# Performance work log

Hardware: AMD Instinct MI355X
Metric: run time of the kernel (lower is better)

The kernel has to match this reference:

```python
import jax, jax.numpy as jnp
import numpy as np

HEADS = 8
DIM_HEAD = 64
DIM = 512
CTX_DIM = 512
INNER = HEADS * DIM_HEAD  # 512
EPS = 1e-5


def layernorm(x, g):
    # repo-style LayerNorm: learnable gain g only, no bias, biased variance
    mean = jnp.mean(x, axis=-1, keepdims=True)
    var = jnp.var(x, axis=-1, keepdims=True)
    return (x - mean) * jax.lax.rsqrt(var + EPS) * g


def setup_inputs() -> dict:
    key = jax.random.key(0)
    ks = jax.random.split(key, 8)
    b, n, m = 2, 4096, 4096
    x = jax.random.normal(ks[0], (b, n, DIM), dtype=jnp.float32)
    context = jax.random.normal(ks[1], (b, m, CTX_DIM), dtype=jnp.float32)
    mask = jax.random.bernoulli(ks[2], 0.9, (b, m))  # bool [b, m]
    # parameters
    g_x = jnp.ones((DIM,), dtype=jnp.float32)
    null_kv = jax.random.normal(ks[3], (2, DIM_HEAD), dtype=jnp.float32)
    Wq = jax.random.normal(ks[4], (DIM, INNER), dtype=jnp.float32) * (DIM ** -0.5)
    Wkv = jax.random.normal(ks[5], (CTX_DIM, 2 * INNER), dtype=jnp.float32) * (CTX_DIM ** -0.5)
    Wo = jax.random.normal(ks[6], (INNER, DIM), dtype=jnp.float32) * (INNER ** -0.5)
    g_out = jnp.ones((DIM,), dtype=jnp.float32)
    return {"x": x, "context": context, "mask": mask, "g_x": g_x,
            "null_kv": null_kv, "Wq": Wq, "Wkv": Wkv, "Wo": Wo, "g_out": g_out}


def reference(x, context, mask, g_x, null_kv, Wq, Wkv, Wo, g_out):
    b, n, _ = x.shape
    m = context.shape[1]
    scale = DIM_HEAD ** (-0.5)  # cosine_sim=False

    xn = layernorm(x, g_x)
    ctx = context  # norm_context=False -> Identity

    q = (xn @ Wq).reshape(b, n, HEADS, DIM_HEAD)          # b n h d
    kv = (ctx @ Wkv).reshape(b, m, 2, HEADS, DIM_HEAD)     # b m 2 h d
    k, v = kv[:, :, 0], kv[:, :, 1]                        # b m h d

    # prepend the null kv token (shared across b, h)
    nk = jnp.broadcast_to(null_kv[0], (b, 1, HEADS, DIM_HEAD))
    nv = jnp.broadcast_to(null_kv[1], (b, 1, HEADS, DIM_HEAD))
    k = jnp.concatenate([nk, k], axis=1)                   # b (m+1) h d
    v = jnp.concatenate([nv, v], axis=1)

    s = jnp.sqrt(jnp.float32(scale))
    q = q * s
    k = k * s

    sim = jnp.einsum('bihd,bjhd->bhij', q, k)              # b h n (m+1)
    max_neg = -jnp.finfo(sim.dtype).max
    full_mask = jnp.pad(mask, ((0, 0), (1, 0)), constant_values=True)  # null token visible
    sim = jnp.where(full_mask[:, None, None, :], sim, max_neg)

    attn = jax.nn.softmax(sim.astype(jnp.float32), axis=-1).astype(sim.dtype)
    out = jnp.einsum('bhij,bjhd->bihd', attn, v).reshape(b, n, INNER)
    out = out @ Wo
    return layernorm(out, g_out)
```

## Files before the change

### kernel.cpp

```cpp
#include <hip/hip_runtime.h>
#include <cfloat>

typedef unsigned short u16;
typedef unsigned int u32;
typedef __bf16 v8bf16 __attribute__((ext_vector_type(8)));
typedef float v4f32 __attribute__((ext_vector_type(4)));
typedef float v16f32 __attribute__((ext_vector_type(16)));

#define MPAD 4224
#define QKS 0.42466090f
#define GRPS 1024

__device__ __forceinline__ u16 f2bf(float f) {
  union { float f; u32 u; } v; v.f = f;
  u32 u = v.u;
  u32 r = (u + 0x7FFFu + ((u >> 16) & 1u)) >> 16;
  return (u16)r;
}

__device__ __forceinline__ u32 pkbf(float lo, float hi) {
  union { float f; u32 u; } a, c;
  a.f = lo; c.f = hi;
  return __builtin_amdgcn_perm(c.u, a.u, 0x07060302);
}

__device__ __forceinline__ float asf(u32 u) {
  union { u32 u; float f; } v; v.u = u; return v.f;
}

__global__ __launch_bounds__(256) void transpose_cast3(const float* __restrict__ Wq,
    const float* __restrict__ Wkv, const float* __restrict__ Wo,
    u16* __restrict__ WqT, u16* __restrict__ WkvT, u16* __restrict__ WoT) {
  __shared__ float tile[32][33];
  int bb = blockIdx.x;
  const float* in; u16* out; int N; float scale; int base;
  if (bb < 256)      { in = Wq;  out = WqT;  N = 512;  scale = QKS; base = bb; }
  else if (bb < 768) { in = Wkv; out = WkvT; N = 1024; scale = 1.f; base = bb - 256; }
  else               { in = Wo;  out = WoT;  N = 512;  scale = 1.f; base = bb - 768; }
  const int K = 512;
  int ntiles = N >> 5;
  int bx = base % ntiles, by = base / ntiles;
  int n0 = bx * 32, k0 = by * 32;
  int c = threadIdx.x & 31, r8 = threadIdx.x >> 5;
#pragma unroll
  for (int i = 0; i < 4; i++) {
    int r = r8 + i * 8;
    tile[r][c] = in[(size_t)(k0 + r) * N + n0 + c];
  }
  __syncthreads();
#pragma unroll
  for (int i = 0; i < 4; i++) {
    int r = r8 + i * 8;
    out[(size_t)(n0 + r) * K + k0 + c] = f2bf(tile[c][r] * scale);
  }
}

__global__ __launch_bounds__(256) void ln_to_bf16(const float* __restrict__ in,
    const float* __restrict__ g, u16* __restrict__ out) {
  int lane = threadIdx.x & 63, w = threadIdx.x >> 6;
  int row = blockIdx.x * 4 + w;
  const float* p = in + (size_t)row * 512 + lane * 8;
  float4 f0 = *(const float4*)p;
  float4 f1 = *(const float4*)(p + 4);
  float v[8] = {f0.x, f0.y, f0.z, f0.w, f1.x, f1.y, f1.z, f1.w};
  float sum = 0.f, sq = 0.f;
#pragma unroll
  for (int i = 0; i < 8; i++) { sum += v[i]; sq += v[i] * v[i]; }
#pragma unroll
  for (int m = 1; m < 64; m <<= 1) { sum += __shfl_xor(sum, m); sq += __shfl_xor(sq, m); }
  float mean = sum * (1.f / 512.f);
  float var = sq * (1.f / 512.f) - mean * mean;
  float rstd = rsqrtf(var + 1e-5f);
  const float* gp = g + lane * 8;
  u16 o[8];
#pragma unroll
  for (int i = 0; i < 8; i++) o[i] = f2bf((v[i] - mean) * rstd * gp[i]);
  *(uint4*)&out[(size_t)row * 512 + lane * 8] = *(uint4*)o;
}

__global__ __launch_bounds__(256) void ln_to_f32(const float* __restrict__ in,
    const float* __restrict__ g, float* __restrict__ out) {
  int lane = threadIdx.x & 63, w = threadIdx.x >> 6;
  int row = blockIdx.x * 4 + w;
  const float* p = in + (size_t)row * 512 + lane * 8;
  float4 f0 = *(const float4*)p;
  float4 f1 = *(const float4*)(p + 4);
  float v[8] = {f0.x, f0.y, f0.z, f0.w, f1.x, f1.y, f1.z, f1.w};
  float sum = 0.f, sq = 0.f;
#pragma unroll
  for (int i = 0; i < 8; i++) { sum += v[i]; sq += v[i] * v[i]; }
#pragma unroll
  for (int m = 1; m < 64; m <<= 1) { sum += __shfl_xor(sum, m); sq += __shfl_xor(sq, m); }
  float mean = sum * (1.f / 512.f);
  float var = sq * (1.f / 512.f) - mean * mean;
  float rstd = rsqrtf(var + 1e-5f);
  const float* gp = g + lane * 8;
  float o[8];
#pragma unroll
  for (int i = 0; i < 8; i++) o[i] = (v[i] - mean) * rstd * gp[i];
  float* q = out + (size_t)row * 512 + lane * 8;
  *(float4*)q = make_float4(o[0], o[1], o[2], o[3]);
  *(float4*)(q + 4) = make_float4(o[4], o[5], o[6], o[7]);
}

__global__ __launch_bounds__(256) void cast_f32_bf16(const float4* __restrict__ in,
    u16* __restrict__ out, int n4) {
  int i = blockIdx.x * 256 + threadIdx.x;
  if (i >= n4) return;
  float4 f = in[i];
  u16 o[4] = {f2bf(f.x), f2bf(f.y), f2bf(f.z), f2bf(f.w)};
  *(uint2*)&out[i * 4] = *(uint2*)o;
}

__global__ void detect_mask_dtype(const unsigned char* __restrict__ m, int* __restrict__ flag) {
  int i = blockIdx.x * 256 + threadIdx.x;
  if (i < 8192 && (i & 3) && m[i]) atomicOr(flag, 1);
}

__global__ void build_maskpad(const void* __restrict__ mask, const int* __restrict__ flag,
    float* __restrict__ mp) {
  int i = blockIdx.x * 256 + threadIdx.x;
  if (i >= 2 * MPAD) return;
  int b = i / MPAD, p = i - b * MPAD;
  float v;
  if (p == 0) v = 0.f;
  else if (p <= 4096) {
    int j = b * 4096 + (p - 1);
    int on = (*flag) ? (((const unsigned char*)mask)[j] != 0)
                     : (((const int*)mask)[j] != 0);
    v = on ? 0.f : -1e38f;
  } else v = -1e38f;
  mp[i] = v;
}

__global__ __launch_bounds__(256) void fill_extras(const float* __restrict__ nullkv,
    u16* __restrict__ KVt) {
  int bh = blockIdx.x, tid = threadIdx.x;
  size_t tb64 = ((size_t)bh * 66 + 64) * 8192;
  uint4 z = make_uint4(0, 0, 0, 0);
  for (int i = tid; i < 2048; i += 256)
    *(uint4*)&KVt[tb64 + (size_t)i * 8] = z;
  size_t tb0 = (size_t)bh * 66 * 8192;
  if (tid < 64) {
    int d = tid;
    KVt[tb0 + (size_t)(d >> 3) * 512 + (d & 7)] = f2bf(nullkv[d] * QKS);
    KVt[tb0 + 4096 + (size_t)d * 8] = f2bf(nullkv[64 + d]);
  }
}

__global__ __launch_bounds__(256) void gemm_bf16(const u16* __restrict__ A,
    const u16* __restrict__ Bt, u16* __restrict__ outb, float* __restrict__ outf,
    u16* __restrict__ KVt, int Ncols, int mode) {
  __shared__ __attribute__((aligned(16))) u16 As[128 * 32];
  __shared__ __attribute__((aligned(16))) u16 Bs[64 * 32];
  int tiles_n = Ncols >> 6;
  int n0 = (blockIdx.x % tiles_n) * 64;
  int m0 = (blockIdx.x / tiles_n) * 128;
  int tid = threadIdx.x;
  int lane = tid & 63, w = tid >> 6, quad = lane >> 4, l15 = lane & 15;
  int srow = tid >> 2, scol = (tid & 3) * 8;
  v4f32 acc[2][4];
#pragma unroll
  for (int i = 0; i < 2; i++)
#pragma unroll
    for (int j = 0; j < 4; j++) acc[i][j] = (v4f32){0.f, 0.f, 0.f, 0.f};

  for (int k0 = 0; k0 < 512; k0 += 32) {
    __syncthreads();
    __builtin_amdgcn_global_load_lds((const u32*)&A[(size_t)(m0 + srow) * 512 + k0 + scol],
                                     (u32*)&As[tid * 8], 16, 0, 0);
    __builtin_amdgcn_global_load_lds((const u32*)&A[(size_t)(m0 + 64 + srow) * 512 + k0 + scol],
                                     (u32*)&As[64 * 32 + tid * 8], 16, 0, 0);
    __builtin_amdgcn_global_load_lds((const u32*)&Bt[(size_t)(n0 + srow) * 512 + k0 + scol],
                                     (u32*)&Bs[tid * 8], 16, 0, 0);
    __syncthreads();
    v8bf16 af[2], bf[4];
#pragma unroll
    for (int i = 0; i < 2; i++)
      af[i] = *(const v8bf16*)&As[(w * 32 + i * 16 + l15) * 32 + quad * 8];
#pragma unroll
    for (int j = 0; j < 4; j++)
      bf[j] = *(const v8bf16*)&Bs[(j * 16 + l15) * 32 + quad * 8];
#pragma unroll
    for (int i = 0; i < 2; i++)
#pragma unroll
      for (int j = 0; j < 4; j++)
        acc[i][j] = __builtin_amdgcn_mfma_f32_16x16x32_bf16(af[i], bf[j], acc[i][j], 0, 0, 0);
  }
#pragma unroll
  for (int i = 0; i < 2; i++) {
    int rbase = m0 + w * 32 + i * 16 + quad * 4;
#pragma unroll
    for (int j = 0; j < 4; j++) {
      int col = n0 + j * 16 + l15;
#pragma unroll
      for (int r = 0; r < 4; r++) {
        float v = acc[i][j][r];
        int row = rbase + r;
        if (mode == 0) {
          outb[(size_t)row * 512 + col] = f2bf(v);
        } else if (mode == 2) {
          outf[(size_t)row * 512 + col] = v;
        } else {
          int b2 = row >> 12, mr = row & 4095;
          int kk = mr + 1, kt = kk >> 6, kl = kk & 63;
          int kvsel = col >> 9, hh = (col >> 6) & 7, d = col & 63;
          size_t tb = ((size_t)(b2 * 8 + hh) * 66 + kt) * 8192;
          if (kvsel == 0) {
            int chunk = (((d >> 4) * 2 + ((d >> 3) & 1)) * 2 + (kl >> 5)) * 32 + (kl & 31);
            KVt[tb + (size_t)chunk * 8 + (d & 7)] = f2bf(v * QKS);
          } else {
            int chunk = (((kl >> 4) * 2 + ((kl >> 3) & 1)) * 2 + (d >> 5)) * 32 + (d & 31);
            KVt[tb + 4096 + (size_t)chunk * 8 + (kl & 7)] = f2bf(v);
          }
        }
      }
    }
  }
}

__global__ __launch_bounds__(256, 2) void attn_kernel(const u16* __restrict__ q,
    const u16* __restrict__ KVt, const float* __restrict__ maskbias,
    u32* __restrict__ Opart, float* __restrict__ lbuf) {
  int bid = blockIdx.x;
  int qt = bid & 15, bhs = bid >> 4;
  int s_p = bhs & 1, bh = bhs >> 1;
  int b = bh >> 3, hh = bh & 7;
  int tid = threadIdx.x, lane = tid & 63, w = tid >> 6;
  int m31 = lane & 31, h = (lane >> 5) & 1;
  int grp = (bh * 16 + qt) * 4 + w;
  int q0 = qt * 256 + w * 64;

  v8bf16 qf[2][4];
#pragma unroll
  for (int qg = 0; qg < 2; qg++) {
    const u16* qp = q + (size_t)(b * 4096 + q0 + qg * 32 + m31) * 512 + hh * 64 + h * 8;
#pragma unroll
    for (int ks = 0; ks < 4; ks++) qf[qg][ks] = *(const v8bf16*)&qp[ks * 16];
  }

  v16f32 acc[2][2];
#pragma unroll
  for (int qg = 0; qg < 2; qg++)
#pragma unroll
    for (int db = 0; db < 2; db++)
#pragma unroll
      for (int i = 0; i < 16; i++) acc[qg][db][i] = 0.f;
  float l_st[2] = {0.f, 0.f};

  const u16* kvb = KVt + (size_t)bh * 66 * 8192 + (size_t)(h * 64 + m31) * 8;
  const float* mg = maskbias + b * MPAD;
  int kt0 = s_p * 33;

  for (int kt = kt0; kt < kt0 + 33; ++kt) {
    const u16* tb = kvb + (size_t)kt * 8192;
    v8bf16 kf[4][2];
#pragma unroll
    for (int ks = 0; ks < 4; ks++)
#pragma unroll
      for (int kc = 0; kc < 2; kc++)
        kf[ks][kc] = *(const v8bf16*)&tb[ks * 1024 + kc * 256];
    v16f32 bias_s[2];
#pragma unroll
    for (int kc = 0; kc < 2; kc++)
#pragma unroll
      for (int gg = 0; gg < 4; gg++) {
        float4 bv = *(const float4*)&mg[kt * 64 + kc * 32 + gg * 8 + h * 4];
        bias_s[kc][gg * 4 + 0] = bv.x;
        bias_s[kc][gg * 4 + 1] = bv.y;
        bias_s[kc][gg * 4 + 2] = bv.z;
        bias_s[kc][gg * 4 + 3] = bv.w;
      }

    v8bf16 pf[2][4];
    {
      v16f32 s[2];
#pragma unroll
      for (int kc = 0; kc < 2; kc++) {
        s[kc] = bias_s[kc];
#pragma unroll
        for (int ks = 0; ks < 4; ks++)
          s[kc] = __builtin_amdgcn_mfma_f32_32x32x16_bf16(kf[ks][kc], qf[0][ks], s[kc], 0, 0, 0);
      }
      float rsum = 0.f;
#pragma unroll
      for (int kc = 0; kc < 2; kc++)
#pragma unroll
        for (int i = 0; i < 16; i++) {
          float pv = __builtin_amdgcn_exp2f(s[kc][i]);
          s[kc][i] = pv;
          rsum += pv;
        }
      rsum += __shfl_xor(rsum, 32);
      l_st[0] += rsum;
#pragma unroll
      for (int kc = 0; kc < 2; kc++)
#pragma unroll
        for (int s16 = 0; s16 < 2; s16++) {
          u32 plo0 = pkbf(s[kc][s16 * 8 + 0], s[kc][s16 * 8 + 1]);
          u32 plo1 = pkbf(s[kc][s16 * 8 + 2], s[kc][s16 * 8 + 3]);
          u32 phi0 = pkbf(s[kc][s16 * 8 + 4], s[kc][s16 * 8 + 5]);
          u32 phi1 = pkbf(s[kc][s16 * 8 + 6], s[kc][s16 * 8 + 7]);
          u32 snd0 = h ? plo0 : phi0;
          u32 snd1 = h ? plo1 : phi1;
          u32 rcv0 = (u32)__shfl_xor((int)snd0, 32);
          u32 rcv1 = (u32)__shfl_xor((int)snd1, 32);
          union { u32 u[4]; v8bf16 v; } pu;
          pu.u[0] = h ? rcv0 : plo0;
          pu.u[1] = h ? rcv1 : plo1;
          pu.u[2] = h ? phi0 : rcv0;
          pu.u[3] = h ? phi1 : rcv1;
          pf[0][kc * 2 + s16] = pu.v;
        }
    }
    {
#pragma unroll
      for (int kc = 0; kc < 2; kc++)
#pragma unroll
        for (int ks = 0; ks < 4; ks++)
          bias_s[kc] = __builtin_amdgcn_mfma_f32_32x32x16_bf16(kf[ks][kc], qf[1][ks], bias_s[kc], 0, 0, 0);
      float rsum = 0.f;
#pragma unroll
      for (int kc = 0; kc < 2; kc++)
#pragma unroll
        for (int i = 0; i < 16; i++) {
          float pv = __builtin_amdgcn_exp2f(bias_s[kc][i]);
          bias_s[kc][i] = pv;
          rsum += pv;
        }
      rsum += __shfl_xor(rsum, 32);
      l_st[1] += rsum;
#pragma unroll
      for (int kc = 0; kc < 2; kc++)
#pragma unroll
        for (int s16 = 0; s16 < 2; s16++) {
          u32 plo0 = pkbf(bias_s[kc][s16 * 8 + 0], bias_s[kc][s16 * 8 + 1]);
          u32 plo1 = pkbf(bias_s[kc][s16 * 8 + 2], bias_s[kc][s16 * 8 + 3]);
          u32 phi0 = pkbf(bias_s[kc][s16 * 8 + 4], bias_s[kc][s16 * 8 + 5]);
          u32 phi1 = pkbf(bias_s[kc][s16 * 8 + 6], bias_s[kc][s16 * 8 + 7]);
          u32 snd0 = h ? plo0 : phi0;
          u32 snd1 = h ? plo1 : phi1;
          u32 rcv0 = (u32)__shfl_xor((int)snd0, 32);
          u32 rcv1 = (u32)__shfl_xor((int)snd1, 32);
          union { u32 u[4]; v8bf16 v; } pu;
          pu.u[0] = h ? rcv0 : plo0;
          pu.u[1] = h ? rcv1 : plo1;
          pu.u[2] = h ? phi0 : rcv0;
          pu.u[3] = h ? phi1 : rcv1;
          pf[1][kc * 2 + s16] = pu.v;
        }
    }

    v8bf16 vf[4][2];
#pragma unroll
    for (int jb = 0; jb < 4; jb++)
#pragma unroll
      for (int db = 0; db < 2; db++)
        vf[jb][db] = *(const v8bf16*)&tb[4096 + jb * 1024 + db * 256];

#pragma unroll
    for (int qg = 0; qg < 2; qg++)
#pragma unroll
      for (int jb = 0; jb < 4; jb++)
#pragma unroll
        for (int db = 0; db < 2; db++)
          acc[qg][db] = __builtin_amdgcn_mfma_f32_32x32x16_bf16(vf[jb][db], pf[qg][jb], acc[qg][db], 0, 0, 0);
  }

  size_t ob = (size_t)(s_p * GRPS + grp) * 2048;
#pragma unroll
  for (int qg = 0; qg < 2; qg++)
#pragma unroll
    for (int db = 0; db < 2; db++)
#pragma unroll
      for (int rp = 0; rp < 8; rp++)
        Opart[ob + qg * 1024 + (size_t)(db * 8 + rp) * 64 + lane] =
            pkbf(acc[qg][db][2 * rp], acc[qg][db][2 * rp + 1]);
  if (h == 0) {
    lbuf[(size_t)(s_p * GRPS + grp) * 64 + m31] = l_st[0];
    lbuf[(size_t)(s_p * GRPS + grp) * 64 + 32 + m31] = l_st[1];
  }
}

__global__ __launch_bounds__(256) void attn_combine(const u32* __restrict__ Opart,
    const float* __restrict__ lbuf, u16* __restrict__ attnO) {
  __shared__ __attribute__((aligned(16))) u16 tl[4][2176];
  int tid = threadIdx.x, lane = tid & 63, w4 = tid >> 6;
  int m31 = lane & 31, h = (lane >> 5) & 1;
  int gq = blockIdx.x * 4 + w4;
  int qg = gq & 1, grp = gq >> 1;
  int w = grp & 3, qt = (grp >> 2) & 15, bh = grp >> 6;
  int b = bh >> 3, hh = bh & 7;

  float l0 = lbuf[(size_t)grp * 64 + qg * 32 + m31];
  float l1 = lbuf[(size_t)(GRPS + grp) * 64 + qg * 32 + m31];
  float inv = 1.f / (l0 + l1);

#pragma unroll
  for (int db = 0; db < 2; db++)
#pragma unroll
    for (int rp = 0; rp < 8; rp++) {
      u32 a = Opart[(size_t)grp * 2048 + qg * 1024 + (db * 8 + rp) * 64 + lane];
      u32 c = Opart[(size_t)(GRPS + grp) * 2048 + qg * 1024 + (db * 8 + rp) * 64 + lane];
      float fe = (asf(a << 16) + asf(c << 16)) * inv;
      float fo = (asf(a & 0xFFFF0000u) + asf(c & 0xFFFF0000u)) * inv;
      int reg = 2 * rp;
      int d0 = (reg & 3) + 8 * (reg >> 2) + 4 * h + 32 * db;
      *(u32*)&tl[w4][m31 * 68 + d0] = pkbf(fe, fo);
    }
  __builtin_amdgcn_s_waitcnt(0);
  int q0 = qt * 256 + w * 64 + qg * 32;
#pragma unroll
  for (int t2 = 0; t2 < 4; t2++) {
    int row = t2 * 8 + (lane >> 3), ch = lane & 7;
    uint4 val = *(uint4*)&tl[w4][row * 68 + ch * 8];
    *(uint4*)&attnO[(size_t)(b * 4096 + q0 + row) * 512 + hh * 64 + ch * 8] = val;
  }
}

extern "C" void kernel_launch(void* const* d_in, const int* in_sizes, int n_in,
                              void* d_out, int out_size, void* d_ws, size_t ws_size,
                              hipStream_t stream) {
  const float* x       = (const float*)d_in[0];
  const float* context = (const float*)d_in[1];
  const void*  mask    = d_in[2];
  const float* g_x     = (const float*)d_in[3];
  const float* null_kv = (const float*)d_in[4];
  const float* Wq      = (const float*)d_in[5];
  const float* Wkv     = (const float*)d_in[6];
  const float* Wo      = (const float*)d_in[7];
  const float* g_out   = (const float*)d_in[8];

  char* w = (char*)d_ws;
  size_t off = 0;
  auto alloc = [&](size_t bytes) { size_t o = off; off = (off + bytes + 255) & ~(size_t)255; return o; };

  u16* WqT    = (u16*)(w + alloc((size_t)512 * 512 * 2));
  u16* WkvT   = (u16*)(w + alloc((size_t)1024 * 512 * 2));
  u16* WoT    = (u16*)(w + alloc((size_t)512 * 512 * 2));
  float* mp   = (float*)(w + alloc((size_t)2 * MPAD * 4));
  int* flag   = (int*)(w + alloc(256));
  u16* KVt    = (u16*)(w + alloc((size_t)16 * 66 * 8192 * 2));
  u16* qb     = (u16*)(w + alloc((size_t)8192 * 512 * 2));
  u16* aO     = (u16*)(w + alloc((size_t)8192 * 512 * 2));
  size_t xn_off = alloc((size_t)8192 * 512 * 2);
  size_t cb_off = alloc((size_t)8192 * 512 * 2);
  float* lbb  = (float*)(w + alloc((size_t)2 * GRPS * 64 * 4));
  u16* xn   = (u16*)(w + xn_off);
  u16* cb   = (u16*)(w + cb_off);
  u32* Opart = (u32*)(w + xn_off);
  float* OP  = (float*)(w + xn_off);

  hipMemsetAsync(flag, 0, 4, stream);
  detect_mask_dtype<<<32, 256, 0, stream>>>((const unsigned char*)mask, flag);
  build_maskpad<<<(2 * MPAD + 255) / 256, 256, 0, stream>>>(mask, flag, mp);

  transpose_cast3<<<1024, 256, 0, stream>>>(Wq, Wkv, Wo, WqT, WkvT, WoT);

  ln_to_bf16<<<2048, 256, 0, stream>>>(x, g_x, xn);
  cast_f32_bf16<<<4096, 256, 0, stream>>>((const float4*)context, cb, 8192 * 512 / 4);
  fill_extras<<<16, 256, 0, stream>>>(null_kv, KVt);

  gemm_bf16<<<(8192 / 128) * (512 / 64), 256, 0, stream>>>(xn, WqT, qb, nullptr, nullptr, 512, 0);
  gemm_bf16<<<(8192 / 128) * (1024 / 64), 256, 0, stream>>>(cb, WkvT, nullptr, nullptr, KVt, 1024, 1);

  attn_kernel<<<512, 256, 0, stream>>>(qb, KVt, mp, Opart, lbb);
  attn_combine<<<512, 256, 0, stream>>>(Opart, lbb, aO);

  gemm_bf16<<<(8192 / 128) * (512 / 64), 256, 0, stream>>>(aO, WoT, nullptr, OP, nullptr, 512, 2);
  ln_to_f32<<<2048, 256, 0, stream>>>(OP, g_out, (float*)d_out);
}
```

Before: 272.9 us.

## Enlarge GEMM tiles, software-pipeline attention K loads, use permlane32 swaps

The GEMM moves from 128x64 to 128x128 tiles with a 2x2 wave layout, which improves reuse of the A and B tiles and halves the block count. The attention loop now prefetches the next K tile and mask bias while it computes the current one. It also interleaves the QK MFMAs for the two query groups with the exp and pack steps. Predicated shfl_xor exchanges are replaced by v_permlane32_swap instructions. Together these aim to hide load latency and cut cross-lane overhead, at the cost of higher register pressure and possible occupancy loss.

```diff
diff --git a/kernel.cpp b/kernel.cpp
--- a/kernel.cpp
+++ b/kernel.cpp
@@ -26,6 +26,34 @@
 
 __device__ __forceinline__ float asf(u32 u) {
   union { u32 u; float f; } v; v.u = u; return v.f;
+}
+
+__device__ __forceinline__ void exppack2(v16f32& sA, v16f32& sB, float& lst,
+                                         v8bf16 pf[4]) {
+  float rsum = 0.f;
+#pragma unroll
+  for (int i = 0; i < 16; i++) { float p = __builtin_amdgcn_exp2f(sA[i]); sA[i] = p; rsum += p; }
+#pragma unroll
+  for (int i = 0; i < 16; i++) { float p = __builtin_amdgcn_exp2f(sB[i]); sB[i] = p; rsum += p; }
+  float a2 = rsum, b2 = rsum;
+  asm("v_permlane32_swap_b32 %0, %1" : "+v"(a2), "+v"(b2));
+  lst += a2 + b2;
+#pragma unroll
+  for (int kc = 0; kc < 2; kc++) {
+    v16f32& s = kc ? sB : sA;
+#pragma unroll
+    for (int s16 = 0; s16 < 2; s16++) {
+      u32 w0 = pkbf(s[s16 * 8 + 0], s[s16 * 8 + 1]);
+      u32 w1 = pkbf(s[s16 * 8 + 2], s[s16 * 8 + 3]);
+      u32 w2 = pkbf(s[s16 * 8 + 4], s[s16 * 8 + 5]);
+      u32 w3 = pkbf(s[s16 * 8 + 6], s[s16 * 8 + 7]);
+      asm("v_permlane32_swap_b32 %0, %1" : "+v"(w0), "+v"(w2));
+      asm("v_permlane32_swap_b32 %0, %1" : "+v"(w1), "+v"(w3));
+      union { u32 u[4]; v8bf16 v; } pu;
+      pu.u[0] = w0; pu.u[1] = w1; pu.u[2] = w2; pu.u[3] = w3;
+      pf[kc * 2 + s16] = pu.v;
+    }
+  }
 }
 
 __global__ __launch_bounds__(256) void transpose_cast3(const float* __restrict__ Wq,
@@ -152,16 +180,17 @@
     const u16* __restrict__ Bt, u16* __restrict__ outb, float* __restrict__ outf,
     u16* __restrict__ KVt, int Ncols, int mode) {
   __shared__ __attribute__((aligned(16))) u16 As[128 * 32];
-  __shared__ __attribute__((aligned(16))) u16 Bs[64 * 32];
-  int tiles_n = Ncols >> 6;
-  int n0 = (blockIdx.x % tiles_n) * 64;
+  __shared__ __attribute__((aligned(16))) u16 Bs[128 * 32];
+  int tiles_n = Ncols >> 7;
+  int n0 = (blockIdx.x % tiles_n) * 128;
   int m0 = (blockIdx.x / tiles_n) * 128;
   int tid = threadIdx.x;
   int lane = tid & 63, w = tid >> 6, quad = lane >> 4, l15 = lane & 15;
+  int wr = w >> 1, wc = w & 1;
   int srow = tid >> 2, scol = (tid & 3) * 8;
-  v4f32 acc[2][4];
-#pragma unroll
-  for (int i = 0; i < 2; i++)
+  v4f32 acc[4][4];
+#pragma unroll
+  for (int i = 0; i < 4; i++)
 #pragma unroll
     for (int j = 0; j < 4; j++) acc[i][j] = (v4f32){0.f, 0.f, 0.f, 0.f};
 
@@ -173,26 +202,28 @@
                                      (u32*)&As[64 * 32 + tid * 8], 16, 0, 0);
     __builtin_amdgcn_global_load_lds((const u32*)&Bt[(size_t)(n0 + srow) * 512 + k0 + scol],
                                      (u32*)&Bs[tid * 8], 16, 0, 0);
+    __builtin_amdgcn_global_load_lds((const u32*)&Bt[(size_t)(n0 + 64 + srow) * 512 + k0 + scol],
+                                     (u32*)&Bs[64 * 32 + tid * 8], 16, 0, 0);
     __syncthreads();
-    v8bf16 af[2], bf[4];
-#pragma unroll
-    for (int i = 0; i < 2; i++)
-      af[i] = *(const v8bf16*)&As[(w * 32 + i * 16 + l15) * 32 + quad * 8];
+    v8bf16 af[4], bf[4];
+#pragma unroll
+    for (int i = 0; i < 4; i++)
+      af[i] = *(const v8bf16*)&As[(wr * 64 + i * 16 + l15) * 32 + quad * 8];
 #pragma unroll
     for (int j = 0; j < 4; j++)
-      bf[j] = *(const v8bf16*)&Bs[(j * 16 + l15) * 32 + quad * 8];
-#pragma unroll
-    for (int i = 0; i < 2; i++)
+      bf[j] = *(const v8bf16*)&Bs[(wc * 64 + j * 16 + l15) * 32 + quad * 8];
+#pragma unroll
+    for (int i = 0; i < 4; i++)
 #pragma unroll
       for (int j = 0; j < 4; j++)
         acc[i][j] = __builtin_amdgcn_mfma_f32_16x16x32_bf16(af[i], bf[j], acc[i][j], 0, 0, 0);
   }
 #pragma unroll
-  for (int i = 0; i < 2; i++) {
-    int rbase = m0 + w * 32 + i * 16 + quad * 4;
+  for (int i = 0; i < 4; i++) {
+    int rbase = m0 + wr * 64 + i * 16 + quad * 4;
 #pragma unroll
     for (int j = 0; j < 4; j++) {
-      int col = n0 + j * 16 + l15;
+      int col = n0 + wc * 64 + j * 16 + l15;
 #pragma unroll
       for (int r = 0; r < 4; r++) {
         float v = acc[i][j][r];
@@ -252,103 +283,36 @@
   const float* mg = maskbias + b * MPAD;
   int kt0 = s_p * 33;
 
+  v8bf16 kf[4][2];
+  v16f32 bs0, bs1;
+  {
+    const u16* tb0 = kvb + (size_t)kt0 * 8192;
+#pragma unroll
+    for (int ks = 0; ks < 4; ks++)
+#pragma unroll
+      for (int kc = 0; kc < 2; kc++)
+        kf[ks][kc] = *(const v8bf16*)&tb0[ks * 1024 + kc * 256];
+#pragma unroll
+    for (int gg = 0; gg < 4; gg++) {
+      float4 b0 = *(const float4*)&mg[kt0 * 64 + gg * 8 + h * 4];
+      float4 b1 = *(const float4*)&mg[kt0 * 64 + 32 + gg * 8 + h * 4];
+      bs0[gg * 4 + 0] = b0.x; bs0[gg * 4 + 1] = b0.y; bs0[gg * 4 + 2] = b0.z; bs0[gg * 4 + 3] = b0.w;
+      bs1[gg * 4 + 0] = b1.x; bs1[gg * 4 + 1] = b1.y; bs1[gg * 4 + 2] = b1.z; bs1[gg * 4 + 3] = b1.w;
+    }
+  }
+
   for (int kt = kt0; kt < kt0 + 33; ++kt) {
     const u16* tb = kvb + (size_t)kt * 8192;
-    v8bf16 kf[4][2];
-#pragma unroll
-    for (int ks = 0; ks < 4; ks++)
-#pragma unroll
-      for (int kc = 0; kc < 2; kc++)
-        kf[ks][kc] = *(const v8bf16*)&tb[ks * 1024 + kc * 256];
-    v16f32 bias_s[2];
-#pragma unroll
-    for (int kc = 0; kc < 2; kc++)
-#pragma unroll
-      for (int gg = 0; gg < 4; gg++) {
-        float4 bv = *(const float4*)&mg[kt * 64 + kc * 32 + gg * 8 + h * 4];
-        bias_s[kc][gg * 4 + 0] = bv.x;
-        bias_s[kc][gg * 4 + 1] = bv.y;
-        bias_s[kc][gg * 4 + 2] = bv.z;
-        bias_s[kc][gg * 4 + 3] = bv.w;
-      }
+    int ktn = (kt + 1 < kt0 + 33) ? kt + 1 : kt0;
+    const u16* tbn = kvb + (size_t)ktn * 8192;
 
     v8bf16 pf[2][4];
-    {
-      v16f32 s[2];
-#pragma unroll
-      for (int kc = 0; kc < 2; kc++) {
-        s[kc] = bias_s[kc];
-#pragma unroll
-        for (int ks = 0; ks < 4; ks++)
-          s[kc] = __builtin_amdgcn_mfma_f32_32x32x16_bf16(kf[ks][kc], qf[0][ks], s[kc], 0, 0, 0);
-      }
-      float rsum = 0.f;
-#pragma unroll
-      for (int kc = 0; kc < 2; kc++)
-#pragma unroll
-        for (int i = 0; i < 16; i++) {
-          float pv = __builtin_amdgcn_exp2f(s[kc][i]);
-          s[kc][i] = pv;
-          rsum += pv;
-        }
-      rsum += __shfl_xor(rsum, 32);
-      l_st[0] += rsum;
-#pragma unroll
-      for (int kc = 0; kc < 2; kc++)
-#pragma unroll
-        for (int s16 = 0; s16 < 2; s16++) {
-          u32 plo0 = pkbf(s[kc][s16 * 8 + 0], s[kc][s16 * 8 + 1]);
-          u32 plo1 = pkbf(s[kc][s16 * 8 + 2], s[kc][s16 * 8 + 3]);
-          u32 phi0 = pkbf(s[kc][s16 * 8 + 4], s[kc][s16 * 8 + 5]);
-          u32 phi1 = pkbf(s[kc][s16 * 8 + 6], s[kc][s16 * 8 + 7]);
-          u32 snd0 = h ? plo0 : phi0;
-          u32 snd1 = h ? plo1 : phi1;
-          u32 rcv0 = (u32)__shfl_xor((int)snd0, 32);
-          u32 rcv1 = (u32)__shfl_xor((int)snd1, 32);
-          union { u32 u[4]; v8bf16 v; } pu;
-          pu.u[0] = h ? rcv0 : plo0;
-          pu.u[1] = h ? rcv1 : plo1;
-          pu.u[2] = h ? phi0 : rcv0;
-          pu.u[3] = h ? phi1 : rcv1;
-          pf[0][kc * 2 + s16] = pu.v;
-        }
-    }
-    {
-#pragma unroll
-      for (int kc = 0; kc < 2; kc++)
-#pragma unroll
-        for (int ks = 0; ks < 4; ks++)
-          bias_s[kc] = __builtin_amdgcn_mfma_f32_32x32x16_bf16(kf[ks][kc], qf[1][ks], bias_s[kc], 0, 0, 0);
-      float rsum = 0.f;
-#pragma unroll
-      for (int kc = 0; kc < 2; kc++)
-#pragma unroll
-        for (int i = 0; i < 16; i++) {
-          float pv = __builtin_amdgcn_exp2f(bias_s[kc][i]);
-          bias_s[kc][i] = pv;
-          rsum += pv;
-        }
-      rsum += __shfl_xor(rsum, 32);
-      l_st[1] += rsum;
-#pragma unroll
-      for (int kc = 0; kc < 2; kc++)
-#pragma unroll
-        for (int s16 = 0; s16 < 2; s16++) {
-          u32 plo0 = pkbf(bias_s[kc][s16 * 8 + 0], bias_s[kc][s16 * 8 + 1]);
-          u32 plo1 = pkbf(bias_s[kc][s16 * 8 + 2], bias_s[kc][s16 * 8 + 3]);
-          u32 phi0 = pkbf(bias_s[kc][s16 * 8 + 4], bias_s[kc][s16 * 8 + 5]);
-          u32 phi1 = pkbf(bias_s[kc][s16 * 8 + 6], bias_s[kc][s16 * 8 + 7]);
-          u32 snd0 = h ? plo0 : phi0;
-          u32 snd1 = h ? plo1 : phi1;
-          u32 rcv0 = (u32)__shfl_xor((int)snd0, 32);
-          u32 rcv1 = (u32)__shfl_xor((int)snd1, 32);
-          union { u32 u[4]; v8bf16 v; } pu;
-          pu.u[0] = h ? rcv0 : plo0;
-          pu.u[1] = h ? rcv1 : plo1;
-          pu.u[2] = h ? phi0 : rcv0;
-          pu.u[3] = h ? phi1 : rcv1;
-          pf[1][kc * 2 + s16] = pu.v;
-        }
+
+    v16f32 s0 = bs0, s1 = bs1;
+#pragma unroll
+    for (int ks = 0; ks < 4; ks++) {
+      s0 = __builtin_amdgcn_mfma_f32_32x32x16_bf16(kf[ks][0], qf[0][ks], s0, 0, 0, 0);
+      s1 = __builtin_amdgcn_mfma_f32_32x32x16_bf16(kf[ks][1], qf[0][ks], s1, 0, 0, 0);
     }
 
     v8bf16 vf[4][2];
@@ -358,6 +322,31 @@
       for (int db = 0; db < 2; db++)
         vf[jb][db] = *(const v8bf16*)&tb[4096 + jb * 1024 + db * 256];
 
+    exppack2(s0, s1, l_st[0], pf[0]);
+
+#pragma unroll
+    for (int ks = 0; ks < 4; ks++) {
+      bs0 = __builtin_amdgcn_mfma_f32_32x32x16_bf16(kf[ks][0], qf[1][ks], bs0, 0, 0, 0);
+      bs1 = __builtin_amdgcn_mfma_f32_32x32x16_bf16(kf[ks][1], qf[1][ks], bs1, 0, 0, 0);
+    }
+
+    v8bf16 kfn[4][2];
+#pragma unroll
+    for (int ks = 0; ks < 4; ks++)
+#pragma unroll
+      for (int kc = 0; kc < 2; kc++)
+        kfn[ks][kc] = *(const v8bf16*)&tbn[ks * 1024 + kc * 256];
+    v16f32 nb0, nb1;
+#pragma unroll
+    for (int gg = 0; gg < 4; gg++) {
+      float4 b0 = *(const float4*)&mg[ktn * 64 + gg * 8 + h * 4];
+      float4 b1 = *(const float4*)&mg[ktn * 64 + 32 + gg * 8 + h * 4];
+      nb0[gg * 4 + 0] = b0.x; nb0[gg * 4 + 1] = b0.y; nb0[gg * 4 + 2] = b0.z; nb0[gg * 4 + 3] = b0.w;
+      nb1[gg * 4 + 0] = b1.x; nb1[gg * 4 + 1] = b1.y; nb1[gg * 4 + 2] = b1.z; nb1[gg * 4 + 3] = b1.w;
+    }
+
+    exppack2(bs0, bs1, l_st[1], pf[1]);
+
 #pragma unroll
     for (int qg = 0; qg < 2; qg++)
 #pragma unroll
@@ -365,6 +354,13 @@
 #pragma unroll
         for (int db = 0; db < 2; db++)
           acc[qg][db] = __builtin_amdgcn_mfma_f32_32x32x16_bf16(vf[jb][db], pf[qg][jb], acc[qg][db], 0, 0, 0);
+
+#pragma unroll
+    for (int ks = 0; ks < 4; ks++)
+#pragma unroll
+      for (int kc = 0; kc < 2; kc++)
+        kf[ks][kc] = kfn[ks][kc];
+    bs0 = nb0; bs1 = nb1;
   }
 
   size_t ob = (size_t)(s_p * GRPS + grp) * 2048;
@@ -461,12 +457,12 @@
   cast_f32_bf16<<<4096, 256, 0, stream>>>((const float4*)context, cb, 8192 * 512 / 4);
   fill_extras<<<16, 256, 0, stream>>>(null_kv, KVt);
 
-  gemm_bf16<<<(8192 / 128) * (512 / 64), 256, 0, stream>>>(xn, WqT, qb, nullptr, nullptr, 512, 0);
-  gemm_bf16<<<(8192 / 128) * (1024 / 64), 256, 0, stream>>>(cb, WkvT, nullptr, nullptr, KVt, 1024, 1);
+  gemm_bf16<<<(8192 / 128) * (512 / 128), 256, 0, stream>>>(xn, WqT, qb, nullptr, nullptr, 512, 0);
+  gemm_bf16<<<(8192 / 128) * (1024 / 128), 256, 0, stream>>>(cb, WkvT, nullptr, nullptr, KVt, 1024, 1);
 
   attn_kernel<<<512, 256, 0, stream>>>(qb, KVt, mp, Opart, lbb);
   attn_combine<<<512, 256, 0, stream>>>(Opart, lbb, aO);
 
-  gemm_bf16<<<(8192 / 128) * (512 / 64), 256, 0, stream>>>(aO, WoT, nullptr, OP, nullptr, 512, 2);
+  gemm_bf16<<<(8192 / 128) * (512 / 128), 256, 0, stream>>>(aO, WoT, nullptr, OP, nullptr, 512, 2);
   ln_to_f32<<<2048, 256, 0, stream>>>(OP, g_out, (float*)d_out);
 }
```

Measured after the change: 278.9 us. 1.02x slower.

## Enlarge GEMM tiles, fuse prep kernels, fold mask detection, remap attention blocks

Applied to the files above, without the earlier changes.

The GEMM tile grows from 128x64 to 128x128, with a 2x2 warp layout and 16 accumulators per warp, so each loaded A tile is reused across more columns and fewer blocks are launched. The x layernorm and the context cast are merged into one launch. Mask dtype detection moves into build_maskpad, which drops a memset and a kernel, though every block now redundantly scans the first 8192 mask bytes. Attention block indices are permuted to spread (batch, head) work across the GPU. The larger tile raises register pressure and leaves only 256 blocks for the 512-column GEMMs, which may underfill the device.

```diff
diff --git a/kernel.cpp b/kernel.cpp
--- a/kernel.cpp
+++ b/kernel.cpp
@@ -55,27 +55,36 @@
   }
 }
 
-__global__ __launch_bounds__(256) void ln_to_bf16(const float* __restrict__ in,
-    const float* __restrict__ g, u16* __restrict__ out) {
-  int lane = threadIdx.x & 63, w = threadIdx.x >> 6;
-  int row = blockIdx.x * 4 + w;
-  const float* p = in + (size_t)row * 512 + lane * 8;
-  float4 f0 = *(const float4*)p;
-  float4 f1 = *(const float4*)(p + 4);
-  float v[8] = {f0.x, f0.y, f0.z, f0.w, f1.x, f1.y, f1.z, f1.w};
-  float sum = 0.f, sq = 0.f;
-#pragma unroll
-  for (int i = 0; i < 8; i++) { sum += v[i]; sq += v[i] * v[i]; }
-#pragma unroll
-  for (int m = 1; m < 64; m <<= 1) { sum += __shfl_xor(sum, m); sq += __shfl_xor(sq, m); }
-  float mean = sum * (1.f / 512.f);
-  float var = sq * (1.f / 512.f) - mean * mean;
-  float rstd = rsqrtf(var + 1e-5f);
-  const float* gp = g + lane * 8;
-  u16 o[8];
-#pragma unroll
-  for (int i = 0; i < 8; i++) o[i] = f2bf((v[i] - mean) * rstd * gp[i]);
-  *(uint4*)&out[(size_t)row * 512 + lane * 8] = *(uint4*)o;
+__global__ __launch_bounds__(256) void ln_and_cast(const float* __restrict__ x,
+    const float* __restrict__ g, u16* __restrict__ xn,
+    const float4* __restrict__ ctx, u16* __restrict__ cb) {
+  int bb = blockIdx.x;
+  if (bb < 2048) {
+    int lane = threadIdx.x & 63, w = threadIdx.x >> 6;
+    int row = bb * 4 + w;
+    const float* p = x + (size_t)row * 512 + lane * 8;
+    float4 f0 = *(const float4*)p;
+    float4 f1 = *(const float4*)(p + 4);
+    float v[8] = {f0.x, f0.y, f0.z, f0.w, f1.x, f1.y, f1.z, f1.w};
+    float sum = 0.f, sq = 0.f;
+#pragma unroll
+    for (int i = 0; i < 8; i++) { sum += v[i]; sq += v[i] * v[i]; }
+#pragma unroll
+    for (int m = 1; m < 64; m <<= 1) { sum += __shfl_xor(sum, m); sq += __shfl_xor(sq, m); }
+    float mean = sum * (1.f / 512.f);
+    float var = sq * (1.f / 512.f) - mean * mean;
+    float rstd = rsqrtf(var + 1e-5f);
+    const float* gp = g + lane * 8;
+    u16 o[8];
+#pragma unroll
+    for (int i = 0; i < 8; i++) o[i] = f2bf((v[i] - mean) * rstd * gp[i]);
+    *(uint4*)&xn[(size_t)row * 512 + lane * 8] = *(uint4*)o;
+  } else {
+    int i = (bb - 2048) * 256 + threadIdx.x;
+    float4 f = ctx[i];
+    u16 o[4] = {f2bf(f.x), f2bf(f.y), f2bf(f.z), f2bf(f.w)};
+    *(uint2*)&cb[(size_t)i * 4] = *(uint2*)o;
+  }
 }
 
 __global__ __launch_bounds__(256) void ln_to_f32(const float* __restrict__ in,
@@ -103,31 +112,31 @@
   *(float4*)(q + 4) = make_float4(o[4], o[5], o[6], o[7]);
 }
 
-__global__ __launch_bounds__(256) void cast_f32_bf16(const float4* __restrict__ in,
-    u16* __restrict__ out, int n4) {
-  int i = blockIdx.x * 256 + threadIdx.x;
-  if (i >= n4) return;
-  float4 f = in[i];
-  u16 o[4] = {f2bf(f.x), f2bf(f.y), f2bf(f.z), f2bf(f.w)};
-  *(uint2*)&out[i * 4] = *(uint2*)o;
-}
-
-__global__ void detect_mask_dtype(const unsigned char* __restrict__ m, int* __restrict__ flag) {
-  int i = blockIdx.x * 256 + threadIdx.x;
-  if (i < 8192 && (i & 3) && m[i]) atomicOr(flag, 1);
-}
-
-__global__ void build_maskpad(const void* __restrict__ mask, const int* __restrict__ flag,
+__global__ __launch_bounds__(256) void build_maskpad(const void* __restrict__ mask,
     float* __restrict__ mp) {
-  int i = blockIdx.x * 256 + threadIdx.x;
+  __shared__ int sflag;
+  int tid = threadIdx.x;
+  if (tid == 0) sflag = 0;
+  __syncthreads();
+  const unsigned char* mb = (const unsigned char*)mask;
+  int loc = 0;
+#pragma unroll
+  for (int k = 0; k < 32; k++) {
+    int i = tid * 32 + k;
+    if ((i & 3) && mb[i]) loc = 1;
+  }
+  if (loc) sflag = 1;
+  __syncthreads();
+  int isbyte = sflag;
+  int i = blockIdx.x * 256 + tid;
   if (i >= 2 * MPAD) return;
   int b = i / MPAD, p = i - b * MPAD;
   float v;
   if (p == 0) v = 0.f;
   else if (p <= 4096) {
     int j = b * 4096 + (p - 1);
-    int on = (*flag) ? (((const unsigned char*)mask)[j] != 0)
-                     : (((const int*)mask)[j] != 0);
+    int on = isbyte ? (((const unsigned char*)mask)[j] != 0)
+                    : (((const int*)mask)[j] != 0);
     v = on ? 0.f : -1e38f;
   } else v = -1e38f;
   mp[i] = v;
@@ -152,16 +161,17 @@
     const u16* __restrict__ Bt, u16* __restrict__ outb, float* __restrict__ outf,
     u16* __restrict__ KVt, int Ncols, int mode) {
   __shared__ __attribute__((aligned(16))) u16 As[128 * 32];
-  __shared__ __attribute__((aligned(16))) u16 Bs[64 * 32];
-  int tiles_n = Ncols >> 6;
-  int n0 = (blockIdx.x % tiles_n) * 64;
+  __shared__ __attribute__((aligned(16))) u16 Bs[128 * 32];
+  int tiles_n = Ncols >> 7;
+  int n0 = (blockIdx.x % tiles_n) * 128;
   int m0 = (blockIdx.x / tiles_n) * 128;
   int tid = threadIdx.x;
   int lane = tid & 63, w = tid >> 6, quad = lane >> 4, l15 = lane & 15;
+  int wr = w >> 1, wc = w & 1;
   int srow = tid >> 2, scol = (tid & 3) * 8;
-  v4f32 acc[2][4];
-#pragma unroll
-  for (int i = 0; i < 2; i++)
+  v4f32 acc[4][4];
+#pragma unroll
+  for (int i = 0; i < 4; i++)
 #pragma unroll
     for (int j = 0; j < 4; j++) acc[i][j] = (v4f32){0.f, 0.f, 0.f, 0.f};
 
@@ -173,26 +183,28 @@
                                      (u32*)&As[64 * 32 + tid * 8], 16, 0, 0);
     __builtin_amdgcn_global_load_lds((const u32*)&Bt[(size_t)(n0 + srow) * 512 + k0 + scol],
                                      (u32*)&Bs[tid * 8], 16, 0, 0);
+    __builtin_amdgcn_global_load_lds((const u32*)&Bt[(size_t)(n0 + 64 + srow) * 512 + k0 + scol],
+                                     (u32*)&Bs[64 * 32 + tid * 8], 16, 0, 0);
     __syncthreads();
-    v8bf16 af[2], bf[4];
-#pragma unroll
-    for (int i = 0; i < 2; i++)
-      af[i] = *(const v8bf16*)&As[(w * 32 + i * 16 + l15) * 32 + quad * 8];
+    v8bf16 af[4], bf[4];
+#pragma unroll
+    for (int i = 0; i < 4; i++)
+      af[i] = *(const v8bf16*)&As[(wr * 64 + i * 16 + l15) * 32 + quad * 8];
 #pragma unroll
     for (int j = 0; j < 4; j++)
-      bf[j] = *(const v8bf16*)&Bs[(j * 16 + l15) * 32 + quad * 8];
-#pragma unroll
-    for (int i = 0; i < 2; i++)
+      bf[j] = *(const v8bf16*)&Bs[(wc * 64 + j * 16 + l15) * 32 + quad * 8];
+#pragma unroll
+    for (int i = 0; i < 4; i++)
 #pragma unroll
       for (int j = 0; j < 4; j++)
         acc[i][j] = __builtin_amdgcn_mfma_f32_16x16x32_bf16(af[i], bf[j], acc[i][j], 0, 0, 0);
   }
 #pragma unroll
-  for (int i = 0; i < 2; i++) {
-    int rbase = m0 + w * 32 + i * 16 + quad * 4;
+  for (int i = 0; i < 4; i++) {
+    int rbase = m0 + wr * 64 + i * 16 + quad * 4;
 #pragma unroll
     for (int j = 0; j < 4; j++) {
-      int col = n0 + j * 16 + l15;
+      int col = n0 + wc * 64 + j * 16 + l15;
 #pragma unroll
       for (int r = 0; r < 4; r++) {
         float v = acc[i][j][r];
@@ -222,7 +234,8 @@
 __global__ __launch_bounds__(256, 2) void attn_kernel(const u16* __restrict__ q,
     const u16* __restrict__ KVt, const float* __restrict__ maskbias,
     u32* __restrict__ Opart, float* __restrict__ lbuf) {
-  int bid = blockIdx.x;
+  int obid = blockIdx.x;
+  int bid = (obid & 7) * 64 + (obid >> 3);
   int qt = bid & 15, bhs = bid >> 4;
   int s_p = bhs & 1, bh = bhs >> 1;
   int b = bh >> 3, hh = bh & 7;
@@ -439,7 +452,6 @@
   u16* WkvT   = (u16*)(w + alloc((size_t)1024 * 512 * 2));
   u16* WoT    = (u16*)(w + alloc((size_t)512 * 512 * 2));
   float* mp   = (float*)(w + alloc((size_t)2 * MPAD * 4));
-  int* flag   = (int*)(w + alloc(256));
   u16* KVt    = (u16*)(w + alloc((size_t)16 * 66 * 8192 * 2));
   u16* qb     = (u16*)(w + alloc((size_t)8192 * 512 * 2));
   u16* aO     = (u16*)(w + alloc((size_t)8192 * 512 * 2));
@@ -451,22 +463,19 @@
   u32* Opart = (u32*)(w + xn_off);
   float* OP  = (float*)(w + xn_off);
 
-  hipMemsetAsync(flag, 0, 4, stream);
-  detect_mask_dtype<<<32, 256, 0, stream>>>((const unsigned char*)mask, flag);
-  build_maskpad<<<(2 * MPAD + 255) / 256, 256, 0, stream>>>(mask, flag, mp);
+  build_maskpad<<<(2 * MPAD + 255) / 256, 256, 0, stream>>>(mask, mp);
 
   transpose_cast3<<<1024, 256, 0, stream>>>(Wq, Wkv, Wo, WqT, WkvT, WoT);
 
-  ln_to_bf16<<<2048, 256, 0, stream>>>(x, g_x, xn);
-  cast_f32_bf16<<<4096, 256, 0, stream>>>((const float4*)context, cb, 8192 * 512 / 4);
+  ln_and_cast<<<6144, 256, 0, stream>>>(x, g_x, xn, (const float4*)context, cb);
   fill_extras<<<16, 256, 0, stream>>>(null_kv, KVt);
 
-  gemm_bf16<<<(8192 / 128) * (512 / 64), 256, 0, stream>>>(xn, WqT, qb, nullptr, nullptr, 512, 0);
-  gemm_bf16<<<(8192 / 128) * (1024 / 64), 256, 0, stream>>>(cb, WkvT, nullptr, nullptr, KVt, 1024, 1);
+  gemm_bf16<<<(8192 / 128) * (512 / 128), 256, 0, stream>>>(xn, WqT, qb, nullptr, nullptr, 512, 0);
+  gemm_bf16<<<(8192 / 128) * (1024 / 128), 256, 0, stream>>>(cb, WkvT, nullptr, nullptr, KVt, 1024, 1);
 
   attn_kernel<<<512, 256, 0, stream>>>(qb, KVt, mp, Opart, lbb);
   attn_combine<<<512, 256, 0, stream>>>(Opart, lbb, aO);
 
-  gemm_bf16<<<(8192 / 128) * (512 / 64), 256, 0, stream>>>(aO, WoT, nullptr, OP, nullptr, 512, 2);
+  gemm_bf16<<<(8192 / 128) * (512 / 128), 256, 0, stream>>>(aO, WoT, nullptr, OP, nullptr, 512, 2);
   ln_to_f32<<<2048, 256, 0, stream>>>(OP, g_out, (float*)d_out);
 }
```

Result: no change. 270.4 us (-0.9%).
